# Kernel tuning notes

Measured on AMD Instinct MI355X. Metric: run time of the kernel, lower is better.

## Reference

```python
import jax, jax.numpy as jnp
import numpy as np

BN_EPS = 1e-5
MIN_DIST = 1e-10

def _three_nn(xyz_up, xyz_down):
    # Pairwise squared distances (B, N, M) via expansion: ||a-b||^2 = |a|^2 + |b|^2 - 2 a.b
    up_sq = jnp.sum(xyz_up * xyz_up, axis=-1, keepdims=True)        # (B, N, 1)
    down_sq = jnp.sum(xyz_down * xyz_down, axis=-1)[:, None, :]      # (B, 1, M)
    cross = jnp.einsum('bnd,bmd->bnm', xyz_up, xyz_down)             # (B, N, M)
    d2 = up_sq + down_sq - 2.0 * cross
    neg_vals, idx = jax.lax.top_k(-d2, 3)                            # 3 smallest dists
    return -neg_vals, idx                                            # (B,N,3), (B,N,3)

def _three_interpolate(features_down, idx, weight):
    # features_down: (B, C, M); idx, weight: (B, N, 3) -> (B, C, N)
    f = jnp.transpose(features_down, (0, 2, 1))                      # (B, M, C)
    gathered = jax.vmap(lambda fm, im: fm[im])(f, idx)               # (B, N, 3, C)
    interp = jnp.einsum('bnkc,bnk->bcn', gathered, weight)           # (B, C, N)
    return interp

def _conv_bn_relu(x, W, gamma, beta):
    # x: (B, C_in, N); W: (C_out, C_in) 1x1 conv, no bias
    y = jnp.einsum('oc,bcn->bon', W, x)
    mean = jnp.mean(y, axis=(0, 2), keepdims=True)
    var = jnp.mean((y - mean) ** 2, axis=(0, 2), keepdims=True)      # biased var (torch BN)
    y = (y - mean) * jax.lax.rsqrt(var + BN_EPS)
    y = y * gamma[None, :, None] + beta[None, :, None]
    return jax.nn.relu(y)

def setup_inputs() -> dict:
    key = jax.random.key(0)
    ks = jax.random.split(key, 8)
    B, N, M = 8, 8192, 2048
    C_down, C_skip = 256, 128
    C_in = C_down + C_skip
    xyz_up = jax.random.normal(ks[0], (B, N, 3), dtype=jnp.float32)
    xyz_down = jax.random.normal(ks[1], (B, M, 3), dtype=jnp.float32)
    features_up = jax.random.normal(ks[2], (B, C_skip, N), dtype=jnp.float32)
    features_down = jax.random.normal(ks[3], (B, C_down, M), dtype=jnp.float32)
    W1 = jax.random.normal(ks[4], (256, C_in), dtype=jnp.float32) * (1.0 / np.sqrt(C_in))
    W2 = jax.random.normal(ks[5], (256, 256), dtype=jnp.float32) * (1.0 / np.sqrt(256))
    g1 = jnp.ones((256,), jnp.float32); b1 = jnp.zeros((256,), jnp.float32)
    g2 = jnp.ones((256,), jnp.float32); b2 = jnp.zeros((256,), jnp.float32)
    return {"xyz_up": xyz_up, "xyz_down": xyz_down, "features_up": features_up,
            "features_down": features_down, "W1": W1, "g1": g1, "b1": b1,
            "W2": W2, "g2": g2, "b2": b2}

def reference(xyz_up, xyz_down, features_up, features_down, W1, g1, b1, W2, g2, b2):
    dist_sq, idx = _three_nn(xyz_up, xyz_down)
    dist_sq = jnp.maximum(dist_sq, MIN_DIST)
    weight = 1.0 / dist_sq
    weight = weight / jnp.sum(weight, axis=-1, keepdims=True)
    interpolated = _three_interpolate(features_down, idx, weight)    # (B, C_down, N)
    combined = jnp.concatenate([interpolated, features_up], axis=1)  # (B, C_in, N)
    h = _conv_bn_relu(combined, W1, g1, b1)
    out = _conv_bn_relu(h, W2, g2, b2)
    return out
```

## Files before the change

### kernel.cpp

```cpp
#include <hip/hip_runtime.h>
#include <hip/hip_bf16.h>

#define NB 8
#define NQ 8192
#define MP 2048
#define CDW 256
#define CSK 128
#define CIN 384
#define COUT 256

typedef __bf16 bf16_t;
typedef bf16_t bf16x8 __attribute__((ext_vector_type(8)));
typedef float f32x4 __attribute__((ext_vector_type(4)));

static __device__ __forceinline__ float bf2f(unsigned short u){
  union { unsigned int ui; float f; } v; v.ui = ((unsigned int)u) << 16; return v.f;
}
static __device__ __forceinline__ unsigned short f2bf(float f){
  union { float f; unsigned int u; } v; v.f = f;
  unsigned int u = v.u;
  return (unsigned short)((u + 0x7FFFu + ((u >> 16) & 1u)) >> 16);
}

__global__ void k_cvt_w(const float* __restrict__ W1, const float* __restrict__ W2,
                        unsigned short* __restrict__ W1b, unsigned short* __restrict__ W2b){
  int i = blockIdx.x * 256 + threadIdx.x;
  if (i < COUT*CIN) W1b[i] = f2bf(W1[i]);
  if (i < COUT*COUT) W2b[i] = f2bf(W2[i]);
}

__global__ __launch_bounds__(256) void k_z(const unsigned short* __restrict__ W1b,
    const float* __restrict__ fd, unsigned short* __restrict__ Z){
  __shared__ unsigned short Bl[64][264];
  int b = blockIdx.y, m0 = blockIdx.x << 6;
  int t = threadIdx.x;
  {
    int m = t & 63, cs0 = t >> 6;
    for (int it = 0; it < 64; ++it){
      int c = cs0 + (it << 2);
      Bl[m][c] = f2bf(fd[((size_t)b*CDW + c)*MP + m0 + m]);
    }
  }
  __syncthreads();
  int l = t & 63, wv = t >> 6;
  int lr = l & 15, lg = l >> 4;
  int ob = wv << 6;
  f32x4 acc[4][4];
  #pragma unroll
  for (int i = 0; i < 4; ++i)
    #pragma unroll
    for (int j = 0; j < 4; ++j)
      acc[i][j] = (f32x4){0.f, 0.f, 0.f, 0.f};
  #pragma unroll 1
  for (int kt = 0; kt < 8; ++kt){
    int k0 = (kt << 5) + (lg << 3);
    bf16x8 af[4], bv[4];
    #pragma unroll
    for (int of = 0; of < 4; ++of)
      af[of] = *(const bf16x8*)(W1b + (size_t)(ob + (of<<4) + lr)*CIN + k0);
    #pragma unroll
    for (int nf = 0; nf < 4; ++nf)
      bv[nf] = *(const bf16x8*)&Bl[(nf<<4) + lr][k0];
    #pragma unroll
    for (int of = 0; of < 4; ++of)
      #pragma unroll
      for (int nf = 0; nf < 4; ++nf)
        acc[of][nf] = __builtin_amdgcn_mfma_f32_16x16x32_bf16(af[of], bv[nf], acc[of][nf], 0, 0, 0);
  }
  #pragma unroll
  for (int of = 0; of < 4; ++of){
    int o = ob + (of<<4) + (lg<<2);
    #pragma unroll
    for (int nf = 0; nf < 4; ++nf){
      int m = m0 + (nf<<4) + lr;
      ushort4 pk;
      pk.x = f2bf(acc[of][nf][0]);
      pk.y = f2bf(acc[of][nf][1]);
      pk.z = f2bf(acc[of][nf][2]);
      pk.w = f2bf(acc[of][nf][3]);
      *(ushort4*)(Z + (((size_t)b*MP + m) << 8) + o) = pk;
    }
  }
}

#define CHUNKS 8
#define MC (MP/CHUNKS)

#define NN_SKIP(P)                                                           \
  asm volatile(                                                              \
      "v_fma_f32 %[s], %[qx], %[px], %[pw]\n\t"                              \
      "v_fma_f32 %[s], %[qy], %[py], %[s]\n\t"                               \
      "v_fma_f32 %[s], %[qz], %[pz], %[s]\n\t"                               \
      "v_cmp_gt_f32 vcc, %[s], %[s2]\n\t"                                    \
      "s_cbranch_vccz L_%=\n\t"                                              \
      "v_cmp_gt_f32 %[m1], %[s], %[s1]\n\t"                                  \
      "v_cmp_gt_f32 %[m0], %[s], %[s0]\n\t"                                  \
      "v_cndmask_b32 %[s2], %[s2], %[s], vcc\n\t"                            \
      "v_cndmask_b32 %[i2], %[i2], %[mi], vcc\n\t"                           \
      "v_cndmask_b32 %[s2], %[s2], %[s1], %[m1]\n\t"                         \
      "v_cndmask_b32 %[i2], %[i2], %[i1], %[m1]\n\t"                         \
      "v_cndmask_b32 %[s1], %[s1], %[s], %[m1]\n\t"                          \
      "v_cndmask_b32 %[i1], %[i1], %[mi], %[m1]\n\t"                         \
      "v_cndmask_b32 %[s1], %[s1], %[s0], %[m0]\n\t"                         \
      "v_cndmask_b32 %[i1], %[i1], %[i0], %[m0]\n\t"                         \
      "v_cndmask_b32 %[s0], %[s0], %[s], %[m0]\n\t"                          \
      "v_cndmask_b32 %[i0], %[i0], %[mi], %[m0]\n\t"                         \
      "L_%=:\n\t"                                                            \
      "v_add_u32 %[mi], 1, %[mi]\n\t"                                        \
      : [s]"=&v"(sv), [m0]"=&s"(mk0), [m1]"=&s"(mk1),                        \
        [s0]"+v"(s0), [s1]"+v"(s1), [s2]"+v"(s2),                            \
        [i0]"+v"(i0), [i1]"+v"(i1), [i2]"+v"(i2), [mi]"+v"(mi)               \
      : [qx]"v"(qx), [qy]"v"(qy), [qz]"v"(qz),                               \
        [px]"v"((P).x), [py]"v"((P).y), [pz]"v"((P).z), [pw]"v"((P).w)       \
      : "vcc")

__global__ __launch_bounds__(256, 2) void k_nn_part(const float* __restrict__ xu, const float* __restrict__ xd,
                                                    float* __restrict__ pd, int* __restrict__ pi){
  int b = blockIdx.z, ch = blockIdx.y, nt = blockIdx.x;
  int t = threadIdx.x;
  __shared__ float4 pts[MC];
  const float* xdb = xd + ((size_t)b*MP + (size_t)ch*MC)*3;
  if (t < MC){
    int p = t;
    float x = xdb[p*3+0], y = xdb[p*3+1], z = xdb[p*3+2];
    pts[p] = make_float4(x, y, z, -0.5f*(x*x + y*y + z*z));
  }
  __syncthreads();
  int n = nt*256 + t;
  const float* q = xu + ((size_t)b*NQ + n)*3;
  float qx = q[0], qy = q[1], qz = q[2];
  float qs = qx*qx + qy*qy + qz*qz;
  float s0 = -3.4e38f, s1 = -3.4e38f, s2 = -3.4e38f;
  int i0 = 0, i1 = 0, i2 = 0, mi = 0;
  float sv;
  unsigned long long mk0, mk1;
  #pragma unroll 1
  for (int mb = 0; mb < MC; mb += 8){
    float4 P0 = pts[mb+0], P1 = pts[mb+1], P2 = pts[mb+2], P3 = pts[mb+3];
    float4 P4 = pts[mb+4], P5 = pts[mb+5], P6 = pts[mb+6], P7 = pts[mb+7];
    NN_SKIP(P0); NN_SKIP(P1); NN_SKIP(P2); NN_SKIP(P3);
    NN_SKIP(P4); NN_SKIP(P5); NN_SKIP(P6); NN_SKIP(P7);
  }
  int gb = ch*MC;
  size_t base = (((size_t)b*CHUNKS + ch)*NQ + n)*3;
  pd[base+0] = qs - 2.f*s0; pd[base+1] = qs - 2.f*s1; pd[base+2] = qs - 2.f*s2;
  pi[base+0] = gb + i0; pi[base+1] = gb + i1; pi[base+2] = gb + i2;
}

__global__ void k_nn_merge(const float* __restrict__ pd, const int* __restrict__ pi,
                           int* __restrict__ idx3, float* __restrict__ w3){
  int gid = blockIdx.x * 256 + threadIdx.x;
  int b = gid >> 13, n = gid & (NQ-1);
  float d0 = 3.4e38f, d1 = 3.4e38f, d2 = 3.4e38f;
  int i0 = 0, i1 = 0, i2 = 0;
  for (int ch = 0; ch < CHUNKS; ++ch){
    size_t base = (((size_t)b*CHUNKS + ch)*NQ + n)*3;
    #pragma unroll
    for (int k = 0; k < 3; ++k){
      float d = pd[base + k]; int gm = pi[base + k];
      bool c0 = d < d0, c1 = d < d1, c2 = d < d2;
      d2 = c1 ? d1 : (c2 ? d : d2);  i2 = c1 ? i1 : (c2 ? gm : i2);
      d1 = c0 ? d0 : (c1 ? d : d1);  i1 = c0 ? i0 : (c1 ? gm : i1);
      d0 = c0 ? d : d0;              i0 = c0 ? gm : i0;
    }
  }
  float w0 = 1.f / fmaxf(d0, 1e-10f);
  float w1 = 1.f / fmaxf(d1, 1e-10f);
  float w2 = 1.f / fmaxf(d2, 1e-10f);
  float s = w0 + w1 + w2;
  idx3[gid*3+0] = i0; idx3[gid*3+1] = i1; idx3[gid*3+2] = i2;
  w3[gid*3+0] = w0/s; w3[gid*3+1] = w1/s; w3[gid*3+2] = w2/s;
}

__global__ __launch_bounds__(256) void k_fused1(const unsigned short* __restrict__ W1b,
    const float* __restrict__ fu, const int* __restrict__ idx3, const float* __restrict__ w3,
    const unsigned short* __restrict__ Z,
    unsigned short* __restrict__ Y1, float* __restrict__ Sp, float* __restrict__ SSp){
  __shared__ unsigned short Xl[64][136];
  int tile = blockIdx.x;
  int b = tile >> 7;
  int n0 = (tile & 127) << 6;
  int t = threadIdx.x;
  {
    int n = t & 63, cs0 = t >> 6;
    for (int it = 0; it < 32; ++it){
      int cs = cs0 + (it << 2);
      Xl[n][cs] = f2bf(fu[((size_t)b*CSK + cs)*NQ + n0 + n]);
    }
  }
  __syncthreads();
  int l = t & 63, wv = t >> 6;
  int lr = l & 15, lg = l >> 4;
  int ob = wv << 6;
  f32x4 acc[4][4];
  #pragma unroll
  for (int i = 0; i < 4; ++i)
    #pragma unroll
    for (int j = 0; j < 4; ++j)
      acc[i][j] = (f32x4){0.f, 0.f, 0.f, 0.f};
  #pragma unroll 1
  for (int kt = 0; kt < 4; ++kt){
    int k0 = (kt << 5) + (lg << 3);
    bf16x8 af[4], bv[4];
    #pragma unroll
    for (int of = 0; of < 4; ++of)
      af[of] = *(const bf16x8*)(W1b + (size_t)(ob + (of<<4) + lr)*CIN + 256 + k0);
    #pragma unroll
    for (int nf = 0; nf < 4; ++nf)
      bv[nf] = *(const bf16x8*)&Xl[(nf<<4) + lr][k0];
    #pragma unroll
    for (int of = 0; of < 4; ++of)
      #pragma unroll
      for (int nf = 0; nf < 4; ++nf)
        acc[of][nf] = __builtin_amdgcn_mfma_f32_16x16x32_bf16(af[of], bv[nf], acc[of][nf], 0, 0, 0);
  }
  const unsigned short* Zb = Z + (((size_t)b*MP) << 8);
  #pragma unroll
  for (int nf = 0; nf < 4; ++nf){
    int nn = n0 + (nf<<4) + lr;
    int q = ((b << 13) + nn) * 3;
    int j0 = idx3[q], j1 = idx3[q+1], j2 = idx3[q+2];
    float w0 = w3[q], w1 = w3[q+1], w2 = w3[q+2];
    const unsigned short* z0p = Zb + ((size_t)j0 << 8);
    const unsigned short* z1p = Zb + ((size_t)j1 << 8);
    const unsigned short* z2p = Zb + ((size_t)j2 << 8);
    #pragma unroll
    for (int of = 0; of < 4; ++of){
      int o = ob + (of<<4) + (lg<<2);
      ushort4 z0 = *(const ushort4*)(z0p + o);
      ushort4 z1 = *(const ushort4*)(z1p + o);
      ushort4 z2 = *(const ushort4*)(z2p + o);
      acc[of][nf][0] += w0*bf2f(z0.x) + w1*bf2f(z1.x) + w2*bf2f(z2.x);
      acc[of][nf][1] += w0*bf2f(z0.y) + w1*bf2f(z1.y) + w2*bf2f(z2.y);
      acc[of][nf][2] += w0*bf2f(z0.z) + w1*bf2f(z1.z) + w2*bf2f(z2.z);
      acc[of][nf][3] += w0*bf2f(z0.w) + w1*bf2f(z1.w) + w2*bf2f(z2.w);
    }
  }
  #pragma unroll
  for (int of = 0; of < 4; ++of){
    int o = ob + (of<<4) + (lg<<2);
    #pragma unroll
    for (int nf = 0; nf < 4; ++nf){
      int n = n0 + (nf<<4) + lr;
      size_t pos = ((size_t)b << 13) + n;
      ushort4 pk;
      pk.x = f2bf(acc[of][nf][0]);
      pk.y = f2bf(acc[of][nf][1]);
      pk.z = f2bf(acc[of][nf][2]);
      pk.w = f2bf(acc[of][nf][3]);
      *(ushort4*)(Y1 + pos*COUT + o) = pk;
    }
  }
  #pragma unroll
  for (int of = 0; of < 4; ++of){
    #pragma unroll
    for (int r = 0; r < 4; ++r){
      float sv = acc[of][0][r] + acc[of][1][r] + acc[of][2][r] + acc[of][3][r];
      float sq = acc[of][0][r]*acc[of][0][r] + acc[of][1][r]*acc[of][1][r]
               + acc[of][2][r]*acc[of][2][r] + acc[of][3][r]*acc[of][3][r];
      #pragma unroll
      for (int off = 1; off < 16; off <<= 1){
        sv += __shfl_xor(sv, off);
        sq += __shfl_xor(sq, off);
      }
      if (lr == 0){
        int o = ob + (of<<4) + (lg<<2) + r;
        Sp[(size_t)tile*256 + o] = sv;
        SSp[(size_t)tile*256 + o] = sq;
      }
    }
  }
}

__global__ __launch_bounds__(256) void k_reduce2(const float* __restrict__ Sp, const float* __restrict__ SSp,
    const float* __restrict__ g, const float* __restrict__ be,
    float* __restrict__ scale, float* __restrict__ shift){
  int t = threadIdx.x;
  int o = blockIdx.x * 4 + (t >> 6);
  int lane = t & 63;
  float s = 0.f, ss = 0.f;
  #pragma unroll
  for (int j = 0; j < 16; ++j){
    size_t row = (size_t)(lane + (j << 6))*256 + o;
    s += Sp[row]; ss += SSp[row];
  }
  #pragma unroll
  for (int off = 1; off < 64; off <<= 1){
    s += __shfl_xor(s, off); ss += __shfl_xor(ss, off);
  }
  if (lane == 0){
    float mean = s / 65536.f;
    float var = ss / 65536.f - mean*mean;
    float inv = rsqrtf(var + 1e-5f);
    float sc = g[o] * inv;
    scale[o] = sc;
    shift[o] = be[o] - mean * sc;
  }
}

__global__ __launch_bounds__(256) void k_gemm2(const unsigned short* __restrict__ W2b,
    const unsigned short* __restrict__ Y1, const float* __restrict__ scale1,
    const float* __restrict__ shift1, unsigned short* __restrict__ Y2,
    float* __restrict__ Sp, float* __restrict__ SSp){
  __shared__ unsigned short buf[256*68];
  int tile = blockIdx.x;
  int b = tile >> 7;
  int n0 = (tile & 127) << 6;
  int t = threadIdx.x;
  {
    int nn0 = t >> 6;
    int cb = (t & 63) << 2;
    float scl[4], shl[4];
    #pragma unroll
    for (int j = 0; j < 4; ++j){ scl[j] = scale1[cb+j]; shl[j] = shift1[cb+j]; }
    for (int it = 0; it < 16; ++it){
      int nn = nn0 + (it << 2);
      size_t pos = ((size_t)b << 13) + n0 + nn;
      ushort4 a = *(const ushort4*)(Y1 + pos*COUT + cb);
      ushort4 r;
      r.x = f2bf(fmaxf(bf2f(a.x)*scl[0] + shl[0], 0.f));
      r.y = f2bf(fmaxf(bf2f(a.y)*scl[1] + shl[1], 0.f));
      r.z = f2bf(fmaxf(bf2f(a.z)*scl[2] + shl[2], 0.f));
      r.w = f2bf(fmaxf(bf2f(a.w)*scl[3] + shl[3], 0.f));
      *(ushort4*)&buf[nn*264 + cb] = r;
    }
  }
  __syncthreads();
  int l = t & 63, wv = t >> 6;
  int lr = l & 15, lg = l >> 4;
  int ob = wv << 6;
  f32x4 acc[4][4];
  #pragma unroll
  for (int i = 0; i < 4; ++i)
    #pragma unroll
    for (int j = 0; j < 4; ++j)
      acc[i][j] = (f32x4){0.f, 0.f, 0.f, 0.f};
  #pragma unroll 1
  for (int kt = 0; kt < 8; ++kt){
    int k0 = (kt << 5) + (lg << 3);
    bf16x8 af[4], bv[4];
    #pragma unroll
    for (int of = 0; of < 4; ++of)
      af[of] = *(const bf16x8*)(W2b + (size_t)(ob + (of<<4) + lr)*COUT + k0);
    #pragma unroll
    for (int nf = 0; nf < 4; ++nf)
      bv[nf] = *(const bf16x8*)&buf[((nf<<4) + lr)*264 + k0];
    #pragma unroll
    for (int of = 0; of < 4; ++of)
      #pragma unroll
      for (int nf = 0; nf < 4; ++nf)
        acc[of][nf] = __builtin_amdgcn_mfma_f32_16x16x32_bf16(af[of], bv[nf], acc[of][nf], 0, 0, 0);
  }
  #pragma unroll
  for (int of = 0; of < 4; ++of){
    #pragma unroll
    for (int r = 0; r < 4; ++r){
      float sv = acc[of][0][r] + acc[of][1][r] + acc[of][2][r] + acc[of][3][r];
      float sq = acc[of][0][r]*acc[of][0][r] + acc[of][1][r]*acc[of][1][r]
               + acc[of][2][r]*acc[of][2][r] + acc[of][3][r]*acc[of][3][r];
      #pragma unroll
      for (int off = 1; off < 16; off <<= 1){
        sv += __shfl_xor(sv, off);
        sq += __shfl_xor(sq, off);
      }
      if (lr == 0){
        int o = ob + (of<<4) + (lg<<2) + r;
        Sp[(size_t)tile*256 + o] = sv;
        SSp[(size_t)tile*256 + o] = sq;
      }
    }
  }
  __syncthreads();
  #pragma unroll
  for (int of = 0; of < 4; ++of){
    int o = ob + (of<<4) + (lg<<2);
    #pragma unroll
    for (int nf = 0; nf < 4; ++nf){
      int n = (nf<<4) + lr;
      #pragma unroll
      for (int r = 0; r < 4; ++r)
        buf[(o + r)*68 + n] = f2bf(acc[of][nf][r]);
    }
  }
  __syncthreads();
  {
    int nx = (t & 31) << 1;
    int og = t >> 5;
    for (int it = 0; it < 32; ++it){
      int o = og + (it << 3);
      unsigned int v = (unsigned int)buf[o*68 + nx] | ((unsigned int)buf[o*68 + nx + 1] << 16);
      *(unsigned int*)(Y2 + (((size_t)b*COUT + o) << 13) + n0 + nx) = v;
    }
  }
}

__global__ void k_out(const unsigned short* __restrict__ Y2,
                      const float* __restrict__ scale2, const float* __restrict__ shift2,
                      float* __restrict__ out){
  size_t i = (size_t)blockIdx.x * 256 + threadIdx.x;
  size_t e = i << 2;
  int o = (int)((e >> 13) & 255);
  ushort4 v = *(const ushort4*)(Y2 + e);
  float sc = scale2[o], sh = shift2[o];
  float4 r;
  r.x = fmaxf(bf2f(v.x)*sc + sh, 0.f);
  r.y = fmaxf(bf2f(v.y)*sc + sh, 0.f);
  r.z = fmaxf(bf2f(v.z)*sc + sh, 0.f);
  r.w = fmaxf(bf2f(v.w)*sc + sh, 0.f);
  *(float4*)(out + e) = r;
}

extern "C" void kernel_launch(void* const* d_in, const int* in_sizes, int n_in,
                              void* d_out, int out_size, void* d_ws, size_t ws_size,
                              hipStream_t stream) {
  (void)in_sizes; (void)n_in; (void)out_size; (void)ws_size;
  const float* xu = (const float*)d_in[0];
  const float* xd = (const float*)d_in[1];
  const float* fu = (const float*)d_in[2];
  const float* fd = (const float*)d_in[3];
  const float* W1 = (const float*)d_in[4];
  const float* g1 = (const float*)d_in[5];
  const float* b1 = (const float*)d_in[6];
  const float* W2 = (const float*)d_in[7];
  const float* g2 = (const float*)d_in[8];
  const float* b2 = (const float*)d_in[9];
  float* out = (float*)d_out;

  char* w = (char*)d_ws;
  size_t off = 0;
  unsigned short* Z   = (unsigned short*)(w + off); off += (size_t)NB*MP*256*2;
  unsigned short* W1b = (unsigned short*)(w + off); off += (size_t)COUT*CIN*2;
  unsigned short* W2b = (unsigned short*)(w + off); off += (size_t)COUT*COUT*2;
  float* pd  = (float*)(w + off); off += (size_t)NB*CHUNKS*NQ*3*4;
  int*   pi  = (int*)(w + off);   off += (size_t)NB*CHUNKS*NQ*3*4;
  int*   idx3= (int*)(w + off);   off += (size_t)NB*NQ*3*4;
  float* w3  = (float*)(w + off); off += (size_t)NB*NQ*3*4;
  unsigned short* Y1 = (unsigned short*)(w + off); off += (size_t)NB*NQ*COUT*2;
  unsigned short* Y2 = (unsigned short*)(w + off); off += (size_t)NB*NQ*COUT*2;
  float* Sp1  = (float*)(w + off); off += (size_t)1024*256*4;
  float* SSp1 = (float*)(w + off); off += (size_t)1024*256*4;
  float* Sp2  = (float*)(w + off); off += (size_t)1024*256*4;
  float* SSp2 = (float*)(w + off); off += (size_t)1024*256*4;
  float* scale1 = (float*)(w + off); off += 256*4;
  float* shift1 = (float*)(w + off); off += 256*4;
  float* scale2 = (float*)(w + off); off += 256*4;
  float* shift2 = (float*)(w + off); off += 256*4;

  k_cvt_w<<<dim3(384), dim3(256), 0, stream>>>(W1, W2, W1b, W2b);
  k_z<<<dim3(32, 8), dim3(256), 0, stream>>>(W1b, fd, Z);
  k_nn_part<<<dim3(32, 8, 8), dim3(256), 0, stream>>>(xu, xd, pd, pi);
  k_nn_merge<<<dim3(256), dim3(256), 0, stream>>>(pd, pi, idx3, w3);
  k_fused1<<<dim3(1024), dim3(256), 0, stream>>>(W1b, fu, idx3, w3, Z, Y1, Sp1, SSp1);
  k_reduce2<<<dim3(64), dim3(256), 0, stream>>>(Sp1, SSp1, g1, b1, scale1, shift1);
  k_gemm2<<<dim3(1024), dim3(256), 0, stream>>>(W2b, Y1, scale1, shift1, Y2, Sp2, SSp2);
  k_reduce2<<<dim3(64), dim3(256), 0, stream>>>(Sp2, SSp2, g2, b2, scale2, shift2);
  k_out<<<dim3(16384), dim3(256), 0, stream>>>(Y2, scale2, shift2, out);
}
```

Before: 188.9 us.

## Stage GEMM tile in LDS and do coalesced Z gather, epilogue, and stats

The skip-feature GEMM result is now written to shared memory first. A second phase then has each thread handle 8 contiguous channels of one query point, doing 16-byte gathers of the three neighbour Z rows, adding them, writing Y1 with 16-byte stores and accumulating BN statistics per channel. Before, each lane did scattered 8-byte gathers laid out by the MFMA fragments. Tile-to-block mapping is interleaved across batches, and the partial-stats buffer grows fourfold, with the reducer taking the tile count as a parameter. This costs extra LDS traffic, two more barriers, a larger LDS footprint and a longer stats reduction.

```diff
diff --git a/kernel.cpp b/kernel.cpp
--- a/kernel.cpp
+++ b/kernel.cpp
@@ -12,6 +12,7 @@
 typedef __bf16 bf16_t;
 typedef bf16_t bf16x8 __attribute__((ext_vector_type(8)));
 typedef float f32x4 __attribute__((ext_vector_type(4)));
+typedef unsigned short ushort8 __attribute__((ext_vector_type(8)));
 
 static __device__ __forceinline__ float bf2f(unsigned short u){
   union { unsigned int ui; float f; } v; v.ui = ((unsigned int)u) << 16; return v.f;
@@ -176,12 +177,16 @@
     const float* __restrict__ fu, const int* __restrict__ idx3, const float* __restrict__ w3,
     const unsigned short* __restrict__ Z,
     unsigned short* __restrict__ Y1, float* __restrict__ Sp, float* __restrict__ SSp){
-  __shared__ unsigned short Xl[64][136];
+  __shared__ unsigned short Yl[64*264];
   int tile = blockIdx.x;
-  int b = tile >> 7;
-  int n0 = (tile & 127) << 6;
+  int b = tile & 7;
+  int n0 = (tile >> 3) << 6;
   int t = threadIdx.x;
+  int l = t & 63, wv = t >> 6;
+  int lr = l & 15, lg = l >> 4;
+  int ob = wv << 6;
   {
+    unsigned short (*Xl)[136] = (unsigned short(*)[136])Yl;
     int n = t & 63, cs0 = t >> 6;
     for (int it = 0; it < 32; ++it){
       int cs = cs0 + (it << 2);
@@ -189,98 +194,98 @@
     }
   }
   __syncthreads();
-  int l = t & 63, wv = t >> 6;
-  int lr = l & 15, lg = l >> 4;
-  int ob = wv << 6;
   f32x4 acc[4][4];
   #pragma unroll
   for (int i = 0; i < 4; ++i)
     #pragma unroll
     for (int j = 0; j < 4; ++j)
       acc[i][j] = (f32x4){0.f, 0.f, 0.f, 0.f};
-  #pragma unroll 1
-  for (int kt = 0; kt < 4; ++kt){
-    int k0 = (kt << 5) + (lg << 3);
-    bf16x8 af[4], bv[4];
-    #pragma unroll
-    for (int of = 0; of < 4; ++of)
-      af[of] = *(const bf16x8*)(W1b + (size_t)(ob + (of<<4) + lr)*CIN + 256 + k0);
-    #pragma unroll
-    for (int nf = 0; nf < 4; ++nf)
-      bv[nf] = *(const bf16x8*)&Xl[(nf<<4) + lr][k0];
-    #pragma unroll
-    for (int of = 0; of < 4; ++of)
+  {
+    unsigned short (*Xl)[136] = (unsigned short(*)[136])Yl;
+    #pragma unroll 1
+    for (int kt = 0; kt < 4; ++kt){
+      int k0 = (kt << 5) + (lg << 3);
+      bf16x8 af[4], bv[4];
+      #pragma unroll
+      for (int of = 0; of < 4; ++of)
+        af[of] = *(const bf16x8*)(W1b + (size_t)(ob + (of<<4) + lr)*CIN + 256 + k0);
       #pragma unroll
       for (int nf = 0; nf < 4; ++nf)
-        acc[of][nf] = __builtin_amdgcn_mfma_f32_16x16x32_bf16(af[of], bv[nf], acc[of][nf], 0, 0, 0);
-  }
-  const unsigned short* Zb = Z + (((size_t)b*MP) << 8);
-  #pragma unroll
-  for (int nf = 0; nf < 4; ++nf){
-    int nn = n0 + (nf<<4) + lr;
-    int q = ((b << 13) + nn) * 3;
-    int j0 = idx3[q], j1 = idx3[q+1], j2 = idx3[q+2];
-    float w0 = w3[q], w1 = w3[q+1], w2 = w3[q+2];
-    const unsigned short* z0p = Zb + ((size_t)j0 << 8);
-    const unsigned short* z1p = Zb + ((size_t)j1 << 8);
-    const unsigned short* z2p = Zb + ((size_t)j2 << 8);
-    #pragma unroll
-    for (int of = 0; of < 4; ++of){
-      int o = ob + (of<<4) + (lg<<2);
-      ushort4 z0 = *(const ushort4*)(z0p + o);
-      ushort4 z1 = *(const ushort4*)(z1p + o);
-      ushort4 z2 = *(const ushort4*)(z2p + o);
-      acc[of][nf][0] += w0*bf2f(z0.x) + w1*bf2f(z1.x) + w2*bf2f(z2.x);
-      acc[of][nf][1] += w0*bf2f(z0.y) + w1*bf2f(z1.y) + w2*bf2f(z2.y);
-      acc[of][nf][2] += w0*bf2f(z0.z) + w1*bf2f(z1.z) + w2*bf2f(z2.z);
-      acc[of][nf][3] += w0*bf2f(z0.w) + w1*bf2f(z1.w) + w2*bf2f(z2.w);
-    }
-  }
+        bv[nf] = *(const bf16x8*)&Xl[(nf<<4) + lr][k0];
+      #pragma unroll
+      for (int of = 0; of < 4; ++of)
+        #pragma unroll
+        for (int nf = 0; nf < 4; ++nf)
+          acc[of][nf] = __builtin_amdgcn_mfma_f32_16x16x32_bf16(af[of], bv[nf], acc[of][nf], 0, 0, 0);
+    }
+  }
+  __syncthreads();
   #pragma unroll
   for (int of = 0; of < 4; ++of){
     int o = ob + (of<<4) + (lg<<2);
     #pragma unroll
     for (int nf = 0; nf < 4; ++nf){
-      int n = n0 + (nf<<4) + lr;
-      size_t pos = ((size_t)b << 13) + n;
+      int nl = (nf<<4) + lr;
       ushort4 pk;
       pk.x = f2bf(acc[of][nf][0]);
       pk.y = f2bf(acc[of][nf][1]);
       pk.z = f2bf(acc[of][nf][2]);
       pk.w = f2bf(acc[of][nf][3]);
-      *(ushort4*)(Y1 + pos*COUT + o) = pk;
-    }
-  }
-  #pragma unroll
-  for (int of = 0; of < 4; ++of){
-    #pragma unroll
-    for (int r = 0; r < 4; ++r){
-      float sv = acc[of][0][r] + acc[of][1][r] + acc[of][2][r] + acc[of][3][r];
-      float sq = acc[of][0][r]*acc[of][0][r] + acc[of][1][r]*acc[of][1][r]
-               + acc[of][2][r]*acc[of][2][r] + acc[of][3][r]*acc[of][3][r];
-      #pragma unroll
-      for (int off = 1; off < 16; off <<= 1){
-        sv += __shfl_xor(sv, off);
-        sq += __shfl_xor(sq, off);
-      }
-      if (lr == 0){
-        int o = ob + (of<<4) + (lg<<2) + r;
-        Sp[(size_t)tile*256 + o] = sv;
-        SSp[(size_t)tile*256 + o] = sq;
-      }
+      *(ushort4*)&Yl[nl*264 + o] = pk;
+    }
+  }
+  __syncthreads();
+  int hw = t >> 5;
+  int c  = t & 31;
+  float sv8[8], sq8[8];
+  #pragma unroll
+  for (int j = 0; j < 8; ++j){ sv8[j] = 0.f; sq8[j] = 0.f; }
+  const unsigned short* Zb = Z + (((size_t)b*MP) << 8);
+  #pragma unroll 2
+  for (int i = 0; i < 8; ++i){
+    int ql = (hw << 3) + i;
+    int n = n0 + ql;
+    int q = ((b << 13) + n) * 3;
+    int j0 = idx3[q], j1 = idx3[q+1], j2 = idx3[q+2];
+    float w0 = w3[q], w1 = w3[q+1], w2 = w3[q+2];
+    ushort8 z0 = *(const ushort8*)(Zb + ((size_t)j0 << 8) + (c << 3));
+    ushort8 z1 = *(const ushort8*)(Zb + ((size_t)j1 << 8) + (c << 3));
+    ushort8 z2 = *(const ushort8*)(Zb + ((size_t)j2 << 8) + (c << 3));
+    ushort8 cur = *(const ushort8*)&Yl[ql*264 + (c << 3)];
+    ushort8 pk;
+    #pragma unroll
+    for (int j = 0; j < 8; ++j){
+      float y = bf2f(cur[j]) + w0*bf2f(z0[j]) + w1*bf2f(z1[j]) + w2*bf2f(z2[j]);
+      sv8[j] += y;
+      sq8[j] += y*y;
+      pk[j] = f2bf(y);
+    }
+    *(ushort8*)(Y1 + ((((size_t)b << 13) + n))*COUT + (c << 3)) = pk;
+  }
+  #pragma unroll
+  for (int j = 0; j < 8; ++j){
+    sv8[j] += __shfl_xor(sv8[j], 32);
+    sq8[j] += __shfl_xor(sq8[j], 32);
+  }
+  if (l < 32){
+    size_t row = (size_t)(tile*4 + wv)*256 + (c << 3);
+    #pragma unroll
+    for (int j = 0; j < 8; ++j){
+      Sp[row + j] = sv8[j];
+      SSp[row + j] = sq8[j];
     }
   }
 }
 
 __global__ __launch_bounds__(256) void k_reduce2(const float* __restrict__ Sp, const float* __restrict__ SSp,
     const float* __restrict__ g, const float* __restrict__ be,
-    float* __restrict__ scale, float* __restrict__ shift){
+    float* __restrict__ scale, float* __restrict__ shift, int nt){
   int t = threadIdx.x;
   int o = blockIdx.x * 4 + (t >> 6);
   int lane = t & 63;
   float s = 0.f, ss = 0.f;
-  #pragma unroll
-  for (int j = 0; j < 16; ++j){
+  int jmax = nt >> 6;
+  for (int j = 0; j < jmax; ++j){
     size_t row = (size_t)(lane + (j << 6))*256 + o;
     s += Sp[row]; ss += SSp[row];
   }
@@ -437,8 +442,8 @@
   float* w3  = (float*)(w + off); off += (size_t)NB*NQ*3*4;
   unsigned short* Y1 = (unsigned short*)(w + off); off += (size_t)NB*NQ*COUT*2;
   unsigned short* Y2 = (unsigned short*)(w + off); off += (size_t)NB*NQ*COUT*2;
-  float* Sp1  = (float*)(w + off); off += (size_t)1024*256*4;
-  float* SSp1 = (float*)(w + off); off += (size_t)1024*256*4;
+  float* Sp1  = (float*)(w + off); off += (size_t)4096*256*4;
+  float* SSp1 = (float*)(w + off); off += (size_t)4096*256*4;
   float* Sp2  = (float*)(w + off); off += (size_t)1024*256*4;
   float* SSp2 = (float*)(w + off); off += (size_t)1024*256*4;
   float* scale1 = (float*)(w + off); off += 256*4;
@@ -451,8 +456,8 @@
   k_nn_part<<<dim3(32, 8, 8), dim3(256), 0, stream>>>(xu, xd, pd, pi);
   k_nn_merge<<<dim3(256), dim3(256), 0, stream>>>(pd, pi, idx3, w3);
   k_fused1<<<dim3(1024), dim3(256), 0, stream>>>(W1b, fu, idx3, w3, Z, Y1, Sp1, SSp1);
-  k_reduce2<<<dim3(64), dim3(256), 0, stream>>>(Sp1, SSp1, g1, b1, scale1, shift1);
+  k_reduce2<<<dim3(64), dim3(256), 0, stream>>>(Sp1, SSp1, g1, b1, scale1, shift1, 4096);
   k_gemm2<<<dim3(1024), dim3(256), 0, stream>>>(W2b, Y1, scale1, shift1, Y2, Sp2, SSp2);
-  k_reduce2<<<dim3(64), dim3(256), 0, stream>>>(Sp2, SSp2, g2, b2, scale2, shift2);
+  k_reduce2<<<dim3(64), dim3(256), 0, stream>>>(Sp2, SSp2, g2, b2, scale2, shift2, 1024);
   k_out<<<dim3(16384), dim3(256), 0, stream>>>(Y2, scale2, shift2, out);
 }
```

After: 182.6 us. 3.3% less time.
